# Kernel tuning notes

Measured on AMD Instinct MI355X. Metric: run time of the kernel, lower is better.

## Reference

```python
import jax, jax.numpy as jnp
import numpy as np

B, T, D = 4, 1024, 1024
H = 16
DH = D // H  # 64
NEG = jnp.float32(-2.0**32 + 1)


def _sinusoid_table(T, D):
    pos = np.arange(T)[:, None]
    i = np.arange(D)[None, :]
    angle = pos / np.power(10000.0, 2.0 * (i // 2) / D)
    tab = np.zeros((T, D))
    tab[:, 0::2] = np.sin(angle[:, 0::2])
    tab[:, 1::2] = np.cos(angle[:, 1::2])
    return jnp.asarray(tab, dtype=jnp.float32)


def setup_inputs() -> dict:
    key = jax.random.key(0)
    ks = jax.random.split(key, 10)
    inp = {
        "queries": jax.random.normal(ks[0], (B, T, D), dtype=jnp.float32),
        "keys": jax.random.normal(ks[1], (B, T, D), dtype=jnp.float32),
        "query_lens": jax.random.randint(ks[2], (B, 1), 1, T + 1),
        "key_lens": jax.random.randint(ks[3], (B, 1), 1, T + 1),
        # learned params
        "pe_q": _sinusoid_table(T, D),
        "pe_k": _sinusoid_table(T, D),
        "W_Query": jax.random.truncated_normal(ks[4], -2.0, 2.0, (D, D), dtype=jnp.float32) * 0.05,
        "W_key": jax.random.truncated_normal(ks[5], -2.0, 2.0, (D, D), dtype=jnp.float32) * 0.05,
        "W_Value": jax.random.truncated_normal(ks[6], -2.0, 2.0, (D, D), dtype=jnp.float32) * 0.05,
        "fw1": jax.random.normal(ks[7], (D, 4 * D), dtype=jnp.float32) * (1.0 / np.sqrt(D)),
        "fw2": jax.random.normal(ks[8], (4 * D, D), dtype=jnp.float32) * (1.0 / np.sqrt(4 * D)),
    }
    return inp


def _forward(queries, keys, pe_q, pe_k, W_Query, W_key, W_Value, fw1, fw2,
             query_lens, key_lens):
    scale = jnp.float32(np.sqrt(D))
    # positional encoding (scale=True). NOTE: source bug preserved —
    # keys tensor is overwritten by key_pe applied to the PE'd queries.
    q_in = queries + pe_q[None] * scale          # [B,T,D]
    k_in = q_in + pe_k[None] * scale             # [B,T,D]

    Q = q_in @ W_Query                           # [B,T,D]
    K = k_in @ W_key                             # [B,T,D]
    V = K @ W_Value                              # NOTE: V projected from projected keys (source quirk)

    def heads(x):  # [B,T,D] -> [H,B,T,DH]
        return x.reshape(B, T, H, DH).transpose(2, 0, 1, 3)

    Qh, Kh, Vh = heads(Q), heads(K), heads(V)
    scores = jnp.einsum("hbqd,hbkd->hbqk", Qh, Kh) / jnp.float32(np.sqrt(DH))

    t = jnp.arange(T)
    kmask = (t[None, :] < key_lens).astype(jnp.float32)    # [B,T]
    qmask = (t[None, :] < query_lens).astype(jnp.float32)  # [B,T]

    scores = jnp.where(kmask[None, :, None, :] == 1.0, scores, NEG)
    # blinding: set diagonal to large negative
    eye = jnp.eye(T, dtype=bool)
    scores = jnp.where(eye[None, None], NEG, scores)

    scores = scores - scores.max(axis=-1, keepdims=True)
    probs = jax.nn.softmax(scores, axis=-1)
    probs = probs * qmask[None, :, :, None]

    out = jnp.einsum("hbqk,hbkd->hbqd", probs, Vh)         # [H,B,T,DH]
    result = out.transpose(1, 2, 0, 3).reshape(B, T, D)
    result = result + q_in                                  # residual uses PE'd queries

    ff = jnp.maximum(result @ fw1, 0.0) @ fw2
    result = result + ff
    return result.mean(axis=1, keepdims=True)               # [B,1,D]


def reference(queries, keys, query_lens, key_lens, pe_q, pe_k,
              W_Query, W_key, W_Value, fw1, fw2):
    return _forward(queries, keys, pe_q, pe_k, W_Query, W_key, W_Value,
                    fw1, fw2, query_lens, key_lens)
```

## Files before the change

kernel.cpp:

```cpp
#include <hip/hip_runtime.h>

#define T_ 1024
#define D_ 1024
#define B_ 4
#define H_ 16
#define DH_ 64
#define M_ (B_*T_)
#define NEG_ (-4294967295.0f)

typedef __attribute__((ext_vector_type(8))) _Float16 f16x8;
typedef __attribute__((ext_vector_type(4))) float f32x4;

__device__ __forceinline__ unsigned short f2h(float f) {
    _Float16 h = (_Float16)f; unsigned short u; __builtin_memcpy(&u, &h, 2); return u;
}
__device__ __forceinline__ float h2f(unsigned short u) {
    _Float16 h; __builtin_memcpy(&h, &u, 2); return (float)h;
}

typedef const unsigned int __attribute__((address_space(1)))* gas_p;
typedef unsigned int __attribute__((address_space(3)))* las_p;
__device__ __forceinline__ void gl_lds16(const void* g, void* l) {
    __builtin_amdgcn_global_load_lds((gas_p)g, (las_p)l, 16, 0, 0);
}

__global__ __launch_bounds__(256) void conv_all(const float* __restrict__ q,
                                                const float* __restrict__ peq,
                                                const float* __restrict__ pek,
                                                const float* __restrict__ Wq,
                                                const float* __restrict__ Wk,
                                                const float* __restrict__ Wv,
                                                const float* __restrict__ fw1,
                                                const int* __restrict__ klv,
                                                unsigned short* __restrict__ A2,
                                                unsigned short* __restrict__ B2,
                                                unsigned short* __restrict__ WvT,
                                                unsigned short* __restrict__ fw1T)
{
    int blk = blockIdx.x;
    if (blk < 8192) {
        int i = blk * 256 + threadIdx.x;
        int m = i >> 8, c4 = (i & 255) << 2;
        int mq = m & 4095;
        if (m >= 4096) {
            int row = m - 4096;
            int kl = klv[row >> 10];
            if (kl > 1 && (row & 1023) >= kl) return;
        }
        float4 qv = *(const float4*)(q + (size_t)mq * D_ + c4);
        float4 p  = *(const float4*)(peq + (size_t)(m & (T_-1)) * D_ + c4);
        ushort4 h;
        if (m < 4096) {
            h.x = f2h(qv.x + 32.f*p.x); h.y = f2h(qv.y + 32.f*p.y);
            h.z = f2h(qv.z + 32.f*p.z); h.w = f2h(qv.w + 32.f*p.w);
        } else {
            float4 pk = *(const float4*)(pek + (size_t)(m & (T_-1)) * D_ + c4);
            h.x = f2h(qv.x + 32.f*(p.x + pk.x)); h.y = f2h(qv.y + 32.f*(p.y + pk.y));
            h.z = f2h(qv.z + 32.f*(p.z + pk.z)); h.w = f2h(qv.w + 32.f*(p.w + pk.w));
        }
        *(ushort4*)(A2 + (size_t)m * 1024 + c4) = h;
        return;
    }
    __shared__ float t[32][33];
    int r = threadIdx.x >> 5, c = threadIdx.x & 31;
    if (blk < 10240) {
        int l = blk - 8192;
        int z = l >> 10, k0 = ((l >> 5) & 31) * 32, n0 = (l & 31) * 32;
        const float* W = z ? Wk : Wq;
        #pragma unroll
        for (int rr = 0; rr < 4; ++rr)
            t[r + 8*rr][c] = W[(size_t)(k0 + r + 8*rr) * 1024 + n0 + c];
        __syncthreads();
        #pragma unroll
        for (int rr = 0; rr < 4; ++rr)
            B2[(size_t)(z * 1024 + n0 + r + 8*rr) * 1024 + k0 + c] = f2h(t[c][r + 8*rr]);
    } else if (blk < 11264) {
        int l = blk - 10240;
        int k0 = (l >> 5) * 32, n0 = (l & 31) * 32;
        #pragma unroll
        for (int rr = 0; rr < 4; ++rr)
            t[r + 8*rr][c] = Wv[(size_t)(k0 + r + 8*rr) * 1024 + n0 + c];
        __syncthreads();
        #pragma unroll
        for (int rr = 0; rr < 4; ++rr)
            WvT[(size_t)(n0 + r + 8*rr) * 1024 + k0 + c] = f2h(t[c][r + 8*rr]);
    } else {
        int l = blk - 11264;
        int k0 = (l >> 7) * 32, n0 = (l & 127) * 32;
        #pragma unroll
        for (int rr = 0; rr < 4; ++rr)
            t[r + 8*rr][c] = fw1[(size_t)(k0 + r + 8*rr) * 4096 + n0 + c];
        __syncthreads();
        #pragma unroll
        for (int rr = 0; rr < 4; ++rr)
            fw1T[(size_t)(n0 + r + 8*rr) * 1024 + k0 + c] = f2h(t[c][r + 8*rr]);
    }
}

template<int BM>
__global__ __launch_bounds__(256) void gemm_mfma(
    const unsigned short* __restrict__ A, int lda,
    const unsigned short* __restrict__ B, int ldb, int K,
    float* __restrict__ outf,
    unsigned short* __restrict__ outh, unsigned short* __restrict__ outh2,
    int N, int flags,
    const int* __restrict__ qlv, const int* __restrict__ klv,
    float* __restrict__ hpart)
{
    constexpr int WN = (BM == 128) ? 2 : 4;
    constexpr int FN = 8 / WN;
    constexpr int NA = BM / 32;
    __shared__ __align__(16) unsigned short As[2][BM * 64];
    __shared__ __align__(16) unsigned short Bs[2][128 * 64];
    __shared__ float hp[4][64];
    const int tid = threadIdx.x;
    const int m0 = blockIdx.y * BM, n0 = blockIdx.x << 7;
    if (flags & 32) {
        if (m0 < 4096) {
            if (n0 >= 1024) return;
            if ((m0 & 1023) >= qlv[m0 >> 10]) return;
        } else {
            if (n0 < 1024) return;
            int kl = klv[(m0 - 4096) >> 10];
            if (kl > 1 && (m0 & 1023) >= kl) return;
        }
    }
    if (flags & 256) {
        int bb = m0 >> 10, kl = klv[bb];
        if (kl > 1 && (m0 & 1023) >= kl) return;
    }
    const int lane = tid & 63, wave = tid >> 6;
    const int wm = (wave / WN) * 64;
    const int wn = (wave % WN) * (128 / WN);
    const int rl = lane & 15, kg = lane >> 4;
    const int rl7 = lane & 7;

    int ca[NA]; const unsigned short* gA[NA];
    #pragma unroll
    for (int i = 0; i < NA; ++i) {
        int c = i * 256 + tid;
        int row = c >> 3, k8 = (c & 7) ^ (row & 7);
        ca[i] = c * 8;
        gA[i] = A + (size_t)(m0 + row) * lda + k8 * 8;
    }
    int cb[4]; const unsigned short* gB[4];
    #pragma unroll
    for (int i = 0; i < 4; ++i) {
        int c = i * 256 + tid;
        int row = c >> 3, k8 = (c & 7) ^ (row & 7);
        cb[i] = c * 8;
        gB[i] = B + (size_t)(n0 + row) * ldb + k8 * 8;
    }

    int aoff[2][4], boff[2][FN];
    #pragma unroll
    for (int tt = 0; tt < 2; ++tt) {
        #pragma unroll
        for (int f = 0; f < 4; ++f)
            aoff[tt][f] = (wm + (f << 4) + rl) * 64 + (((tt * 4 + kg) ^ rl7) << 3);
        #pragma unroll
        for (int f = 0; f < FN; ++f)
            boff[tt][f] = (wn + (f << 4) + rl) * 64 + (((tt * 4 + kg) ^ rl7) << 3);
    }

    f32x4 acc[4][FN];
    #pragma unroll
    for (int i = 0; i < 4; ++i)
        #pragma unroll
        for (int j = 0; j < FN; ++j) {
            acc[i][j][0] = 0.f; acc[i][j][1] = 0.f;
            acc[i][j][2] = 0.f; acc[i][j][3] = 0.f;
        }

    const int NT = K >> 6;
    #pragma unroll
    for (int i = 0; i < 4; ++i)  gl_lds16(gB[i], &Bs[0][cb[i]]);
    #pragma unroll
    for (int i = 0; i < NA; ++i) gl_lds16(gA[i], &As[0][ca[i]]);
    #pragma unroll
    for (int i = 0; i < 4; ++i)  gl_lds16(gB[i] + 64, &Bs[1][cb[i]]);
    #pragma unroll
    for (int i = 0; i < NA; ++i) gl_lds16(gA[i] + 64, &As[1][ca[i]]);

    for (int t = 0; t < NT; ++t) {
        const int cur = t & 1;
        if (t + 1 < NT) {
            if constexpr (BM == 128) asm volatile("s_waitcnt vmcnt(8)" ::: "memory");
            else                     asm volatile("s_waitcnt vmcnt(6)" ::: "memory");
        } else {
            asm volatile("s_waitcnt vmcnt(0)" ::: "memory");
        }
        __builtin_amdgcn_s_barrier();
        __builtin_amdgcn_sched_barrier(0);
        f16x8 av[2][4], bv[2][FN];
        #pragma unroll
        for (int tt = 0; tt < 2; ++tt) {
            #pragma unroll
            for (int f = 0; f < 4; ++f)
                av[tt][f] = *(const f16x8*)&As[cur][aoff[tt][f]];
            #pragma unroll
            for (int f = 0; f < FN; ++f)
                bv[tt][f] = *(const f16x8*)&Bs[cur][boff[tt][f]];
        }
        asm volatile("s_waitcnt lgkmcnt(0)" ::: "memory");
        __builtin_amdgcn_sched_barrier(0);
        __builtin_amdgcn_s_barrier();
        __builtin_amdgcn_sched_barrier(0);
        if (t + 2 < NT) {
            const int ko = (t + 2) << 6;
            #pragma unroll
            for (int i = 0; i < 4; ++i)  gl_lds16(gB[i] + ko, &Bs[cur][cb[i]]);
            #pragma unroll
            for (int i = 0; i < NA; ++i) gl_lds16(gA[i] + ko, &As[cur][ca[i]]);
        }
        #pragma unroll
        for (int fm = 0; fm < 4; ++fm)
            #pragma unroll
            for (int fn = 0; fn < FN; ++fn) {
                acc[fm][fn] = __builtin_amdgcn_mfma_f32_16x16x32_f16(av[0][fm], bv[0][fn], acc[fm][fn], 0, 0, 0);
                acc[fm][fn] = __builtin_amdgcn_mfma_f32_16x16x32_f16(av[1][fm], bv[1][fn], acc[fm][fn], 0, 0, 0);
            }
    }

    if (flags & 128) {
        if constexpr (BM == 128) {
            #pragma unroll
            for (int fn = 0; fn < FN; ++fn) {
                float p = 0.f;
                #pragma unroll
                for (int fm = 0; fm < 4; ++fm)
                    #pragma unroll
                    for (int r = 0; r < 4; ++r) p += fmaxf(acc[fm][fn][r], 0.f);
                p += __shfl_xor(p, 16);
                p += __shfl_xor(p, 32);
                if (kg == 0) hp[wave][fn * 16 + rl] = p;
            }
            __syncthreads();
            if (tid < 128) {
                int c = tid;
                float s = (c < 64) ? (hp[0][c] + hp[2][c]) : (hp[1][c - 64] + hp[3][c - 64]);
                hpart[(size_t)blockIdx.y * 4096 + n0 + c] = s;
            }
        }
        return;
    }

    #pragma unroll
    for (int fm = 0; fm < 4; ++fm) {
        int row = m0 + wm + (fm << 4) + (kg << 2);
        #pragma unroll
        for (int fn = 0; fn < FN; ++fn) {
            int col = n0 + wn + (fn << 4) + rl;
            if (flags & 64) {
                ushort4 u;
                u.x = f2h(acc[fm][fn][0]); u.y = f2h(acc[fm][fn][1]);
                u.z = f2h(acc[fm][fn][2]); u.w = f2h(acc[fm][fn][3]);
                size_t a = ((size_t)((row >> 10) * 16 + (col >> 6)) * 64 + (col & 63)) * 1024 + (row & 1023);
                *(ushort4*)(outh + a) = u;
                continue;
            }
            #pragma unroll
            for (int r = 0; r < 4; ++r) {
                float x = acc[fm][fn][r];
                int rr = row + r;
                if (flags & 32) {
                    if (rr < 4096) outh[(size_t)rr * 1024 + col] = f2h(x);
                    else           outh2[(size_t)(rr - 4096) * 1024 + (col - 1024)] = f2h(x);
                } else {
                    size_t idx = (size_t)rr * N + col;
                    if (flags & 1)  x = fmaxf(x, 0.f);
                    if (flags & 8)  outf[idx] = x;
                    if (flags & 16) outh[idx] = f2h(x);
                }
            }
        }
    }
}

__global__ __launch_bounds__(256) void attn_mfma(
    const unsigned short* __restrict__ Qh,
    const unsigned short* __restrict__ Kh,
    const unsigned short* __restrict__ Vt,
    unsigned short* __restrict__ q16,
    const int* __restrict__ qlens, const int* __restrict__ klens)
{
    __shared__ __align__(16) unsigned short KS[2][4096];
    __shared__ __align__(16) unsigned short VtS[2][4096];
    __shared__ __align__(16) unsigned short Pl[4][1152];

    const int tid = threadIdx.x;
    const int bh = blockIdx.x & 63;
    const int qt = blockIdx.x >> 6;
    const int b = bh >> 4, h = bh & 15;
    const int qbase = qt * 64;
    const int qlen = qlens[b], klen = klens[b];
    if (qbase >= qlen) return;

    const int lane = tid & 63, wq = tid >> 6;
    const int rl = lane & 15, kg = lane >> 4, rl7 = lane & 7;
    const int gq = qbase + wq * 16 + rl;

    f16x8 qb[2];
    {
        const unsigned short* p1 = Qh + (size_t)(b * 1024 + gq) * 1024 + h * 64 + kg * 8;
        qb[0] = *(const f16x8*)p1;  qb[1] = *(const f16x8*)(p1 + 32);
    }

    const unsigned short* gK[2]; const unsigned short* gV[2];
    int cs[2];
    #pragma unroll
    for (int i = 0; i < 2; ++i) {
        int c = i * 256 + tid;
        int row = c >> 3, ch = (c & 7) ^ (row & 7);
        cs[i] = c * 8;
        gK[i] = Kh + (size_t)(b * 1024 + row) * 1024 + h * 64 + ch * 8;
        gV[i] = Vt + (size_t)(bh * 64 + row) * 1024 + ch * 8;
    }

    int akoff[4][2];
    #pragma unroll
    for (int mf = 0; mf < 4; ++mf)
        #pragma unroll
        for (int kh = 0; kh < 2; ++kh)
            akoff[mf][kh] = (mf * 16 + rl) * 64 + (((kg + 4 * kh) ^ rl7) << 3);

    f32x4 o[4];
    #pragma unroll
    for (int i = 0; i < 4; ++i) { o[i][0]=0.f; o[i][1]=0.f; o[i][2]=0.f; o[i][3]=0.f; }
    float m_run = -3.0e38f, l_run = 0.f;
    const int nt = (klen == 1) ? (T_ / 64) : ((klen + 63) >> 6);

    gl_lds16(gK[0], &KS[0][cs[0]]);
    gl_lds16(gK[1], &KS[0][cs[1]]);
    gl_lds16(gV[0], &VtS[0][cs[0]]);
    gl_lds16(gV[1], &VtS[0][cs[1]]);
    gl_lds16(gK[0] + 65536, &KS[1][cs[0]]);
    gl_lds16(gK[1] + 65536, &KS[1][cs[1]]);
    gl_lds16(gV[0] + 64,    &VtS[1][cs[0]]);
    gl_lds16(gV[1] + 64,    &VtS[1][cs[1]]);

    for (int kb = 0; kb < nt; ++kb) {
        const int cur = kb & 1;
        const int kbase = kb * 64;
        if (kb + 1 < nt) asm volatile("s_waitcnt vmcnt(4)" ::: "memory");
        else             asm volatile("s_waitcnt vmcnt(0)" ::: "memory");
        __builtin_amdgcn_s_barrier();
        __builtin_amdgcn_sched_barrier(0);

        float v[4][4];
        __builtin_amdgcn_s_setprio(1);
        #pragma unroll
        for (int mf = 0; mf < 4; ++mf) {
            f32x4 s; s[0]=0.f; s[1]=0.f; s[2]=0.f; s[3]=0.f;
            f16x8 a0 = *(const f16x8*)&KS[cur][akoff[mf][0]];
            f16x8 a1 = *(const f16x8*)&KS[cur][akoff[mf][1]];
            s = __builtin_amdgcn_mfma_f32_16x16x32_f16(a0, qb[0], s, 0, 0, 0);
            s = __builtin_amdgcn_mfma_f32_16x16x32_f16(a1, qb[1], s, 0, 0, 0);
            #pragma unroll
            for (int r = 0; r < 4; ++r) {
                int gk = kbase + mf * 16 + kg * 4 + r;
                float x = s[r] * 0.125f;
                if (gk >= klen || gk == gq) x = NEG_;
                v[mf][r] = x;
            }
        }
        __builtin_amdgcn_s_setprio(0);
        float mt = -3.0e38f;
        #pragma unroll
        for (int mf = 0; mf < 4; ++mf)
            #pragma unroll
            for (int r = 0; r < 4; ++r) mt = fmaxf(mt, v[mf][r]);
        mt = fmaxf(mt, __shfl_xor(mt, 16));
        mt = fmaxf(mt, __shfl_xor(mt, 32));
        float mnew = fmaxf(m_run, mt);
        float fac = __expf(m_run - mnew);
        float sum = 0.f;
        #pragma unroll
        for (int mf = 0; mf < 4; ++mf) {
            ushort4 pb;
            pb.x = f2h(__expf(v[mf][0] - mnew));
            pb.y = f2h(__expf(v[mf][1] - mnew));
            pb.z = f2h(__expf(v[mf][2] - mnew));
            pb.w = f2h(__expf(v[mf][3] - mnew));
            sum += h2f(pb.x) + h2f(pb.y) + h2f(pb.z) + h2f(pb.w);
            *(ushort4*)&Pl[wq][rl * 72 + mf * 16 + kg * 4] = pb;
        }
        sum += __shfl_xor(sum, 16);
        sum += __shfl_xor(sum, 32);
        l_run = l_run * fac + sum;
        m_run = mnew;
        #pragma unroll
        for (int i = 0; i < 4; ++i) {
            o[i][0] *= fac; o[i][1] *= fac; o[i][2] *= fac; o[i][3] *= fac;
        }
        f16x8 bp0 = *(const f16x8*)&Pl[wq][rl * 72 + kg * 8];
        f16x8 bp1 = *(const f16x8*)&Pl[wq][rl * 72 + 32 + kg * 8];
        __builtin_amdgcn_s_setprio(1);
        #pragma unroll
        for (int dmf = 0; dmf < 4; ++dmf) {
            f16x8 a0 = *(const f16x8*)&VtS[cur][akoff[dmf][0]];
            f16x8 a1 = *(const f16x8*)&VtS[cur][akoff[dmf][1]];
            o[dmf] = __builtin_amdgcn_mfma_f32_16x16x32_f16(a0, bp0, o[dmf], 0, 0, 0);
            o[dmf] = __builtin_amdgcn_mfma_f32_16x16x32_f16(a1, bp1, o[dmf], 0, 0, 0);
        }
        __builtin_amdgcn_s_setprio(0);
        __builtin_amdgcn_s_barrier();
        __builtin_amdgcn_sched_barrier(0);
        if (kb + 2 < nt) {
            const size_t ko = (size_t)(kbase + 128) * 1024;
            gl_lds16(gK[0] + ko, &KS[cur][cs[0]]);
            gl_lds16(gK[1] + ko, &KS[cur][cs[1]]);
            gl_lds16(gV[0] + kbase + 128, &VtS[cur][cs[0]]);
            gl_lds16(gV[1] + kbase + 128, &VtS[cur][cs[1]]);
        }
    }

    float invl = (gq < qlen) ? (1.f / l_run) : 0.f;
    #pragma unroll
    for (int dmf = 0; dmf < 4; ++dmf)
        #pragma unroll
        for (int r = 0; r < 4; ++r) {
            int dh = dmf * 16 + kg * 4 + r;
            size_t a = (size_t)(b * 1024 + gq) * 1024 + h * 64 + dh;
            q16[a] = f2h(o[dmf][r] * invl + h2f(q16[a]));
        }
}

__global__ __launch_bounds__(256) void mean16(const unsigned short* __restrict__ X,
                                              float* __restrict__ out, int Xdim)
{
    __shared__ float red[4][128];
    int tid = threadIdx.x;
    int b = blockIdx.y;
    int dbase = blockIdx.x * 128;
    int tq = tid >> 6, dd = tid & 63;
    int d = dbase + dd * 2;
    const unsigned short* p = X + ((size_t)b * T_ + tq * 256) * Xdim + d;
    float s0 = 0.f, s1 = 0.f;
    for (int t = 0; t < 256; ++t) {
        ushort2 v = *(const ushort2*)(p + (size_t)t * Xdim);
        s0 += h2f(v.x); s1 += h2f(v.y);
    }
    red[tq][dd*2] = s0; red[tq][dd*2 + 1] = s1;
    __syncthreads();
    if (tq == 0) {
        float a = red[0][dd*2] + red[1][dd*2] + red[2][dd*2] + red[3][dd*2];
        float c = red[0][dd*2+1] + red[1][dd*2+1] + red[2][dd*2+1] + red[3][dd*2+1];
        out[(size_t)b * Xdim + d]     = a * (1.f/1024.f);
        out[(size_t)b * Xdim + d + 1] = c * (1.f/1024.f);
    }
}

__global__ __launch_bounds__(256) void final_partial(const float* __restrict__ Hpart,
                                                     const float* __restrict__ fw2,
                                                     float* __restrict__ Pout)
{
    __shared__ float red[4][4][64];
    __shared__ float hm[4][128];
    int tid = threadIdx.x;
    #pragma unroll
    for (int s = 0; s < 2; ++s) {
        int idx = s * 256 + tid;
        int bb = idx >> 7, jl = idx & 127;
        int j = blockIdx.y * 128 + jl;
        float acc = 0.f;
        #pragma unroll
        for (int i = 0; i < 8; ++i)
            acc += Hpart[((size_t)(bb * 8 + i)) * 4096 + j];
        hm[bb][jl] = acc * (1.f / 1024.f);
    }
    __syncthreads();
    int dd = tid & 63;
    int d = blockIdx.x * 64 + dd;
    int jq = tid >> 6;
    float s4[4] = {0.f, 0.f, 0.f, 0.f};
    for (int jj = 0; jj < 32; ++jj) {
        int jl = jq * 32 + jj;
        int j = blockIdx.y * 128 + jl;
        float wv = fw2[(size_t)j * 1024 + d];
        s4[0] += hm[0][jl] * wv;
        s4[1] += hm[1][jl] * wv;
        s4[2] += hm[2][jl] * wv;
        s4[3] += hm[3][jl] * wv;
    }
    #pragma unroll
    for (int bb = 0; bb < 4; ++bb) red[jq][bb][dd] = s4[bb];
    __syncthreads();
    if (jq == 0) {
        #pragma unroll
        for (int bb = 0; bb < 4; ++bb) {
            float tot = red[0][bb][dd] + red[1][bb][dd] + red[2][bb][dd] + red[3][bb][dd];
            Pout[((size_t)blockIdx.y * 4 + bb) * 1024 + d] = tot;
        }
    }
}

__global__ __launch_bounds__(256) void reduce_out(const float* __restrict__ Mres,
                                                  const float* __restrict__ Pout,
                                                  float* __restrict__ out)
{
    int idx = blockIdx.x * 256 + threadIdx.x;
    int b = idx >> 10, d = idx & 1023;
    float s = Mres[(size_t)b * 1024 + d];
    #pragma unroll
    for (int jy = 0; jy < 32; ++jy)
        s += Pout[((size_t)jy * 4 + b) * 1024 + d];
    out[(size_t)b * 1024 + d] = s;
}

extern "C" void kernel_launch(void* const* d_in, const int* in_sizes, int n_in,
                              void* d_out, int out_size, void* d_ws, size_t ws_size,
                              hipStream_t stream)
{
    const float* queries = (const float*)d_in[0];
    const int*   qlens   = (const int*)d_in[2];
    const int*   klens   = (const int*)d_in[3];
    const float* pe_q    = (const float*)d_in[4];
    const float* pe_k    = (const float*)d_in[5];
    const float* Wq      = (const float*)d_in[6];
    const float* Wk      = (const float*)d_in[7];
    const float* Wv      = (const float*)d_in[8];
    const float* fw1     = (const float*)d_in[9];
    const float* fw2     = (const float*)d_in[10];
    float* out = (float*)d_out;

    char* w = (char*)d_ws;
    unsigned short* Qh   = (unsigned short*)(w);
    unsigned short* A2   = (unsigned short*)(w + (8ll  << 20));
    unsigned short* q16  = A2;
    unsigned short* Kh16 = (unsigned short*)(w + (24ll << 20));
    unsigned short* B2   = (unsigned short*)(w + (32ll << 20));
    unsigned short* WvT  = (unsigned short*)(w + (36ll << 20));
    unsigned short* Vt   = (unsigned short*)(w + (38ll << 20));
    unsigned short* fw1T = (unsigned short*)(w + (46ll << 20));
    float*          Hpart= (float*)(w + (54ll << 20));
    float*          Mres = (float*)(w + (55ll << 20));
    float*          Pout = (float*)(w + (56ll << 20));

    conv_all<<<15360, 256, 0, stream>>>(queries, pe_q, pe_k, Wq, Wk, Wv, fw1, klens,
                                        A2, B2, WvT, fw1T);
    gemm_mfma<128><<<dim3(16, 64), 256, 0, stream>>>(
        A2, 1024, B2, 1024, 1024,
        nullptr, Qh, Kh16, 2048, 32, qlens, klens, nullptr);
    gemm_mfma<64><<<dim3(8, 64), 256, 0, stream>>>(
        Kh16, 1024, WvT, 1024, 1024,
        nullptr, Vt, nullptr, 1024, 64 | 256, nullptr, klens, nullptr);
    attn_mfma<<<1024, 256, 0, stream>>>(Qh, Kh16, Vt, q16, qlens, klens);
    gemm_mfma<128><<<dim3(32, 32), 256, 0, stream>>>(
        q16, 1024, fw1T, 1024, 1024,
        nullptr, nullptr, nullptr, 4096, 128, nullptr, nullptr, Hpart);
    mean16<<<dim3(8, 4), 256, 0, stream>>>(q16, Mres, 1024);
    final_partial<<<dim3(16, 32), 256, 0, stream>>>(Hpart, fw2, Pout);
    reduce_out<<<16, 256, 0, stream>>>(Mres, Pout, out);
}
```

Before: 129.6 us.

## Add dedicated 256x256-tile 8-wave kernel for FFN1 relu-sum GEMM

Replaces the generic 128x128-tile gemm_mfma path for the FFN1 GEMM with a specialized kernel. It uses 512 threads and 256x256 output tiles with swizzled LDS, double-buffered global_load_lds prefetch interleaved with MFMA groups, and s_setprio around the MFMA bursts. Larger tiles raise data reuse per LDS load and halve the number of Hpart row partials, so final_partial now sums 4 partials instead of 8. The cost is much higher register pressure with 32 accumulators per thread, a grid of only 256 blocks which may underfill the GPU, and removal of the now-unused generic epilogue flags.

```diff
diff --git a/kernel.cpp b/kernel.cpp
--- a/kernel.cpp
+++ b/kernel.cpp
@@ -101,18 +101,15 @@
 __global__ __launch_bounds__(256) void gemm_mfma(
     const unsigned short* __restrict__ A, int lda,
     const unsigned short* __restrict__ B, int ldb, int K,
-    float* __restrict__ outf,
     unsigned short* __restrict__ outh, unsigned short* __restrict__ outh2,
     int N, int flags,
-    const int* __restrict__ qlv, const int* __restrict__ klv,
-    float* __restrict__ hpart)
+    const int* __restrict__ qlv, const int* __restrict__ klv)
 {
     constexpr int WN = (BM == 128) ? 2 : 4;
     constexpr int FN = 8 / WN;
     constexpr int NA = BM / 32;
     __shared__ __align__(16) unsigned short As[2][BM * 64];
     __shared__ __align__(16) unsigned short Bs[2][128 * 64];
-    __shared__ float hp[4][64];
     const int tid = threadIdx.x;
     const int m0 = blockIdx.y * BM, n0 = blockIdx.x << 7;
     if (flags & 32) {
@@ -222,29 +219,6 @@
             }
     }
 
-    if (flags & 128) {
-        if constexpr (BM == 128) {
-            #pragma unroll
-            for (int fn = 0; fn < FN; ++fn) {
-                float p = 0.f;
-                #pragma unroll
-                for (int fm = 0; fm < 4; ++fm)
-                    #pragma unroll
-                    for (int r = 0; r < 4; ++r) p += fmaxf(acc[fm][fn][r], 0.f);
-                p += __shfl_xor(p, 16);
-                p += __shfl_xor(p, 32);
-                if (kg == 0) hp[wave][fn * 16 + rl] = p;
-            }
-            __syncthreads();
-            if (tid < 128) {
-                int c = tid;
-                float s = (c < 64) ? (hp[0][c] + hp[2][c]) : (hp[1][c - 64] + hp[3][c - 64]);
-                hpart[(size_t)blockIdx.y * 4096 + n0 + c] = s;
-            }
-        }
-        return;
-    }
-
     #pragma unroll
     for (int fm = 0; fm < 4; ++fm) {
         int row = m0 + wm + (fm << 4) + (kg << 2);
@@ -266,14 +240,123 @@
                 if (flags & 32) {
                     if (rr < 4096) outh[(size_t)rr * 1024 + col] = f2h(x);
                     else           outh2[(size_t)(rr - 4096) * 1024 + (col - 1024)] = f2h(x);
-                } else {
-                    size_t idx = (size_t)rr * N + col;
-                    if (flags & 1)  x = fmaxf(x, 0.f);
-                    if (flags & 8)  outf[idx] = x;
-                    if (flags & 16) outh[idx] = f2h(x);
+                } else if (flags & 16) {
+                    outh[(size_t)rr * N + col] = f2h(x);
                 }
             }
         }
+    }
+}
+
+__global__ __launch_bounds__(512, 2) void ffn1_8p(
+    const unsigned short* __restrict__ A,
+    const unsigned short* __restrict__ B,
+    float* __restrict__ hpart)
+{
+    __shared__ __align__(16) unsigned short As[2][16384];
+    __shared__ __align__(16) unsigned short Bs[2][16384];
+    __shared__ float hp[8][64];
+    const int tid = threadIdx.x;
+    const int m0 = blockIdx.y << 8, n0 = blockIdx.x << 8;
+    const int lane = tid & 63, wave = tid >> 6;
+    const int wm = wave >> 2, wn = wave & 3;
+    const int rl = lane & 15, kg = lane >> 4, rl7 = lane & 7;
+
+    const int row0 = tid >> 3;
+    const int k8c = (tid & 7) ^ (row0 & 7);
+    const int cs0 = tid * 8;
+    const int gofs = row0 * 1024 + k8c * 8;
+    const unsigned short* Ap = A + (size_t)m0 * 1024 + gofs;
+    const unsigned short* Bp = B + (size_t)n0 * 1024 + gofs;
+
+    const int base_a = ((wm * 128 + rl) * 8 + (kg ^ rl7)) * 8;
+    const int base_b = (((wn >> 1) * 128 + (wn & 1) * 64 + rl) * 8 + (kg ^ rl7)) * 8;
+
+    f32x4 acc[8][4];
+    #pragma unroll
+    for (int i = 0; i < 8; ++i)
+        #pragma unroll
+        for (int j = 0; j < 4; ++j) {
+            acc[i][j][0] = 0.f; acc[i][j][1] = 0.f;
+            acc[i][j][2] = 0.f; acc[i][j][3] = 0.f;
+        }
+
+    const int NT = 16;
+    #pragma unroll
+    for (int i = 0; i < 4; ++i) gl_lds16(Ap + i * 65536, &As[0][cs0 + i * 4096]);
+    #pragma unroll
+    for (int i = 0; i < 4; ++i) gl_lds16(Bp + i * 65536, &Bs[0][cs0 + i * 4096]);
+    #pragma unroll
+    for (int i = 0; i < 4; ++i) gl_lds16(Ap + i * 65536 + 64, &As[1][cs0 + i * 4096]);
+    #pragma unroll
+    for (int i = 0; i < 4; ++i) gl_lds16(Bp + i * 65536 + 64, &Bs[1][cs0 + i * 4096]);
+
+    for (int t = 0; t < NT; ++t) {
+        const int cur = t & 1;
+        if (t + 1 < NT) asm volatile("s_waitcnt vmcnt(8)" ::: "memory");
+        else            asm volatile("s_waitcnt vmcnt(0)" ::: "memory");
+        __builtin_amdgcn_s_barrier();
+        __builtin_amdgcn_sched_barrier(0);
+        f16x8 av[8][2], bv[4][2];
+        #pragma unroll
+        for (int f = 0; f < 8; ++f) {
+            int o = base_a + f * 1024;
+            av[f][0] = *(const f16x8*)&As[cur][o];
+            av[f][1] = *(const f16x8*)&As[cur][o ^ 32];
+        }
+        #pragma unroll
+        for (int fn = 0; fn < 4; ++fn) {
+            int o = base_b + fn * 1024;
+            bv[fn][0] = *(const f16x8*)&Bs[cur][o];
+            bv[fn][1] = *(const f16x8*)&Bs[cur][o ^ 32];
+        }
+        asm volatile("s_waitcnt lgkmcnt(0)" ::: "memory");
+        __builtin_amdgcn_sched_barrier(0);
+        __builtin_amdgcn_s_barrier();
+        __builtin_amdgcn_sched_barrier(0);
+        const bool pre = (t + 2 < NT);
+        const int ko = (t + 2) << 6;
+        #pragma unroll
+        for (int p = 0; p < 4; ++p) {
+            if (pre) {
+                if (p < 2) {
+                    gl_lds16(Ap + (2*p) * 65536 + ko,     &As[cur][cs0 + (2*p) * 4096]);
+                    gl_lds16(Ap + (2*p + 1) * 65536 + ko, &As[cur][cs0 + (2*p + 1) * 4096]);
+                } else {
+                    gl_lds16(Bp + (2*p - 4) * 65536 + ko, &Bs[cur][cs0 + (2*p - 4) * 4096]);
+                    gl_lds16(Bp + (2*p - 3) * 65536 + ko, &Bs[cur][cs0 + (2*p - 3) * 4096]);
+                }
+            }
+            __builtin_amdgcn_sched_barrier(0);
+            __builtin_amdgcn_s_setprio(1);
+            #pragma unroll
+            for (int f = 2 * p; f < 2 * p + 2; ++f)
+                #pragma unroll
+                for (int fn = 0; fn < 4; ++fn) {
+                    acc[f][fn] = __builtin_amdgcn_mfma_f32_16x16x32_f16(av[f][0], bv[fn][0], acc[f][fn], 0, 0, 0);
+                    acc[f][fn] = __builtin_amdgcn_mfma_f32_16x16x32_f16(av[f][1], bv[fn][1], acc[f][fn], 0, 0, 0);
+                }
+            __builtin_amdgcn_s_setprio(0);
+            __builtin_amdgcn_sched_barrier(0);
+        }
+    }
+
+    #pragma unroll
+    for (int fn = 0; fn < 4; ++fn) {
+        float p = 0.f;
+        #pragma unroll
+        for (int f = 0; f < 8; ++f)
+            #pragma unroll
+            for (int r = 0; r < 4; ++r) p += fmaxf(acc[f][fn][r], 0.f);
+        p += __shfl_xor(p, 16);
+        p += __shfl_xor(p, 32);
+        if (kg == 0) hp[wave][fn * 16 + rl] = p;
+    }
+    __syncthreads();
+    if (tid < 256) {
+        int wn2 = tid >> 6, cc = tid & 63;
+        float s = hp[wn2][cc] + hp[wn2 + 4][cc];
+        hpart[(size_t)blockIdx.y * 4096 + n0 + wn2 * 64 + cc] = s;
     }
 }
 
@@ -465,8 +548,8 @@
         int j = blockIdx.y * 128 + jl;
         float acc = 0.f;
         #pragma unroll
-        for (int i = 0; i < 8; ++i)
-            acc += Hpart[((size_t)(bb * 8 + i)) * 4096 + j];
+        for (int i = 0; i < 4; ++i)
+            acc += Hpart[((size_t)(bb * 4 + i)) * 4096 + j];
         hm[bb][jl] = acc * (1.f / 1024.f);
     }
     __syncthreads();
@@ -541,14 +624,12 @@
                                         A2, B2, WvT, fw1T);
     gemm_mfma<128><<<dim3(16, 64), 256, 0, stream>>>(
         A2, 1024, B2, 1024, 1024,
-        nullptr, Qh, Kh16, 2048, 32, qlens, klens, nullptr);
+        Qh, Kh16, 2048, 32, qlens, klens);
     gemm_mfma<64><<<dim3(8, 64), 256, 0, stream>>>(
         Kh16, 1024, WvT, 1024, 1024,
-        nullptr, Vt, nullptr, 1024, 64 | 256, nullptr, klens, nullptr);
+        Vt, nullptr, 1024, 64 | 256, nullptr, klens);
     attn_mfma<<<1024, 256, 0, stream>>>(Qh, Kh16, Vt, q16, qlens, klens);
-    gemm_mfma<128><<<dim3(32, 32), 256, 0, stream>>>(
-        q16, 1024, fw1T, 1024, 1024,
-        nullptr, nullptr, nullptr, 4096, 128, nullptr, nullptr, Hpart);
+    ffn1_8p<<<dim3(16, 16), 512, 0, stream>>>(q16, fw1T, Hpart);
     mean16<<<dim3(8, 4), 256, 0, stream>>>(q16, Mres, 1024);
     final_partial<<<dim3(16, 32), 256, 0, stream>>>(Hpart, fw2, Pout);
     reduce_out<<<16, 256, 0, stream>>>(Mres, Pout, out);
```

Result: faster. 125.3 us (-3.3%).
